# Optimization experiments

Hardware: AMD Instinct MI355X
Metric: run time of the kernel (lower is better)

The kernel has to match this reference:

```python
import jax, jax.numpy as jnp
import numpy as np

# ---- HashGrid config (tcnn defaults from module __init__) ----
N_LEVELS = 6
F = 2                      # n_features_per_level
T = 2 ** 19                # hashmap size
BASE = 16                  # base_resolution, per_level_scale=2.0
_RES = [BASE * (2 ** l) for l in range(N_LEVELS)]          # 16..512
_SIZES = [min(r ** 3, T) for r in _RES]                    # dense if grid fits
_OFFSETS = [0] + list(np.cumsum(_SIZES))
TOTAL_ENTRIES = int(_OFFSETS[-1])
_PRIMES = (1, 2654435761, 805459861)
BOX_R = 1.0
DIM_H = 64
DIM_IN = 3 + N_LEVELS * F


def hash_encode(xn, grid):
    """Multi-res hash-grid encoding. xn: [N,3] in [0,1]; grid: [TOTAL_ENTRIES, F]."""
    feats = []
    for l in range(N_LEVELS):
        res, size, off = _RES[l], _SIZES[l], _OFFSETS[l]
        dense = (res ** 3) <= T
        pos = xn * jnp.float32(res - 1) + 0.5          # tcnn: scale*x + 0.5
        pg = jnp.floor(pos)
        frac = pos - pg                                # [N,3]
        pgi = pg.astype(jnp.uint32)
        acc = jnp.zeros((xn.shape[0], F), xn.dtype)
        for corner in range(8):                        # trilinear, 8 corners
            cb = jnp.array([(corner >> d) & 1 for d in range(3)], dtype=jnp.uint32)
            c = pgi + cb                               # [N,3] corner coords
            w = jnp.prod(jnp.where(cb == 1, frac, 1.0 - frac), axis=-1)  # [N]
            if dense:
                c = jnp.minimum(c, jnp.uint32(res - 1))
                idx = c[:, 0] + c[:, 1] * jnp.uint32(res) + c[:, 2] * jnp.uint32(res * res)
            else:
                idx = ((c[:, 0] * jnp.uint32(_PRIMES[0]))
                       ^ (c[:, 1] * jnp.uint32(_PRIMES[1]))
                       ^ (c[:, 2] * jnp.uint32(_PRIMES[2]))) % jnp.uint32(size)
            acc = acc + w[:, None] * grid[jnp.uint32(off) + idx]
        feats.append(acc)
    return jnp.concatenate(feats, axis=-1)             # [N, 12]


def setup_inputs() -> dict:
    key = jax.random.key(0)
    k0, k1, k2 = jax.random.split(key, 3)
    N = 2_097_152
    x = jax.random.uniform(k0, (N, 3), jnp.float32, -1.0, 1.0)
    grid = jax.random.uniform(k1, (TOTAL_ENTRIES, F), jnp.float32, -1e-2, 1e-2)
    W0 = jax.random.normal(k2, (DIM_IN, DIM_H), jnp.float32) * float(np.sqrt(2.0 / DIM_H))
    b0 = jnp.zeros((DIM_H,), jnp.float32)
    W1 = jnp.full((DIM_H, 1), float(np.sqrt(np.pi / DIM_H)), jnp.float32)
    b1 = jnp.full((1,), -1.0, jnp.float32)             # -init_radius
    return {"x": x, "grid": grid, "W0": W0, "b0": b0, "W1": W1, "b1": b1}


def reference(x, grid, W0, b0, W1, b1):
    xn = (x + BOX_R) / (2.0 * BOX_R)                   # normalize to [0,1]
    f = hash_encode(xn, grid)                          # [N,12]
    h = jnp.concatenate([x, f], axis=-1)               # [N,15]
    h = jax.nn.relu(h @ W0 + b0)                       # [N,64]
    return h @ W1 + b1                                 # [N,1] scalar level s
```

## Files before the change

kernel.cpp:

```cpp
#include <hip/hip_runtime.h>


#define HP1 2654435761u
#define HP2 805459861u
#define HMASK ((1u << 19) - 1u)

typedef float v2f __attribute__((ext_vector_type(2)));

static __device__ __forceinline__ unsigned umin_(unsigned a, unsigned b) {
    return a < b ? a : b;
}

static __device__ __forceinline__ unsigned f2bf(float f) {
    unsigned u = __float_as_uint(f);
    return (u + 0x7fffu + ((u >> 16) & 1u)) >> 16;
}
static __device__ __forceinline__ float bf2f_lo(unsigned p) {
    return __uint_as_float((p & 0xffffu) << 16);
}
static __device__ __forceinline__ float bf2f_hi(unsigned p) {
    return __uint_as_float(p & 0xffff0000u);
}

static __device__ __forceinline__ v2f vmax0(v2f s) {
#if __has_builtin(__builtin_elementwise_max)
    return __builtin_elementwise_max(s, (v2f)0.0f);
#else
    v2f r; r.x = fmaxf(s.x, 0.0f); r.y = fmaxf(s.y, 0.0f); return r;
#endif
}

static __device__ __forceinline__ void hash_body(
    const float* __restrict__ x, const float2* __restrict__ tab,
    unsigned* __restrict__ feat, float scale, int N, int bid)
{
    const int gid = bid * 256 + threadIdx.x;
    if (gid >= N) return;

    const float px = __builtin_nontemporal_load(x + 3 * gid + 0);
    const float py = __builtin_nontemporal_load(x + 3 * gid + 1);
    const float pz = __builtin_nontemporal_load(x + 3 * gid + 2);

    const float p0 = fmaf((px + 1.0f) * 0.5f, scale, 0.5f);
    const float p1 = fmaf((py + 1.0f) * 0.5f, scale, 0.5f);
    const float p2 = fmaf((pz + 1.0f) * 0.5f, scale, 0.5f);
    const float g0 = floorf(p0), g1 = floorf(p1), g2 = floorf(p2);
    const float f0 = p0 - g0, f1 = p1 - g1, f2 = p2 - g2;
    const unsigned i0 = (unsigned)g0, i1 = (unsigned)g1, i2 = (unsigned)g2;

    const float wx[2] = {1.0f - f0, f0};
    const float wy[2] = {1.0f - f1, f1};
    const float wz[2] = {1.0f - f2, f2};
    const unsigned hx[2] = {i0, i0 + 1u};
    const unsigned hy[2] = {i1 * HP1, (i1 + 1u) * HP1};
    const unsigned hz[2] = {i2 * HP2, (i2 + 1u) * HP2};

    unsigned idx[8];
    float w[8];
    #pragma unroll
    for (int c = 0; c < 8; ++c) {
        const int bx = c & 1, by = (c >> 1) & 1, bz = (c >> 2) & 1;
        idx[c] = (hx[bx] ^ hy[by] ^ hz[bz]) & HMASK;
        w[c] = wx[bx] * wy[by] * wz[bz];
    }
    float2 v[8];
    #pragma unroll
    for (int c = 0; c < 8; ++c) v[c] = tab[idx[c]];

    float a0 = 0.0f, a1 = 0.0f;
    #pragma unroll
    for (int c = 0; c < 8; ++c) {
        a0 = fmaf(w[c], v[c].x, a0);
        a1 = fmaf(w[c], v[c].y, a1);
    }
    __builtin_nontemporal_store(f2bf(a0) | (f2bf(a1) << 16), feat + gid);
}

__global__ __launch_bounds__(256) void hash3_prep_kernel(
    const float* __restrict__ x, const float2* __restrict__ gtab,
    unsigned* __restrict__ feat0, int N,
    float* __restrict__ wt, unsigned* __restrict__ packed,
    const float* __restrict__ W0, const float* __restrict__ b0,
    const float* __restrict__ W1, const float* __restrict__ b1)
{
    const int nh = (int)gridDim.x - 64;
    if ((int)blockIdx.x >= nh) {
        const int pb = (int)blockIdx.x - nh;
        for (int t = pb * 256 + threadIdx.x; t < 36864; t += 64 * 256) {
            const float2 e = gtab[t];
            packed[t] = f2bf(e.x) | (f2bf(e.y) << 16);
        }
        if (pb == 0) {
            for (int t = threadIdx.x; t < 1024; t += 256) {
                const int j = t >> 4, i = t & 15;
                wt[t] = (i == 15) ? b0[j] : W0[i * 64 + j];
            }
            if (threadIdx.x < 64) wt[1024 + threadIdx.x] = W1[threadIdx.x];
            if (threadIdx.x == 0) wt[1088] = b1[0];
        }
        return;
    }
    hash_body(x, gtab + 299008u, feat0, 127.0f, N, (int)blockIdx.x);
}

__global__ __launch_bounds__(256) void hash_level_kernel(
    const float* __restrict__ x, const float2* __restrict__ tab,
    unsigned* __restrict__ feat, float scale, int N)
{
    hash_body(x, tab, feat, scale, N, (int)blockIdx.x);
}

static __device__ __forceinline__ void dense_level(
    const float2* __restrict__ tab, unsigned res,
    float xn0, float xn1, float xn2, float& o0, float& o1)
{
    const float scale = (float)(res - 1);
    const float p0 = fmaf(xn0, scale, 0.5f);
    const float p1 = fmaf(xn1, scale, 0.5f);
    const float p2 = fmaf(xn2, scale, 0.5f);
    const float g0 = floorf(p0), g1 = floorf(p1), g2 = floorf(p2);
    const float f0 = p0 - g0, f1 = p1 - g1, f2 = p2 - g2;
    const unsigned i0 = (unsigned)g0, i1 = (unsigned)g1, i2 = (unsigned)g2;

    const unsigned rm1 = res - 1u;
    const unsigned cx[2] = {umin_(i0, rm1), umin_(i0 + 1u, rm1)};
    const unsigned cy[2] = {umin_(i1, rm1) * res, umin_(i1 + 1u, rm1) * res};
    const unsigned cz[2] = {umin_(i2, rm1) * res * res,
                            umin_(i2 + 1u, rm1) * res * res};
    const float wx[2] = {1.0f - f0, f0};
    const float wy[2] = {1.0f - f1, f1};
    const float wz[2] = {1.0f - f2, f2};

    float a0 = 0.0f, a1 = 0.0f;
    #pragma unroll
    for (int c = 0; c < 8; ++c) {
        const int bx = c & 1, by = (c >> 1) & 1, bz = (c >> 2) & 1;
        const unsigned idx = cx[bx] + cy[by] + cz[bz];
        const float w = wx[bx] * wy[by] * wz[bz];
        const float2 v = tab[idx];
        a0 = fmaf(w, v.x, a0);
        a1 = fmaf(w, v.y, a1);
    }
    o0 = a0;
    o1 = a1;
}

static __device__ __forceinline__ void dense_level_lds(
    const unsigned* __restrict__ sPk, unsigned off, unsigned res,
    float xn0, float xn1, float xn2, float& o0, float& o1)
{
    const float scale = (float)(res - 1);
    const float p0 = fmaf(xn0, scale, 0.5f);
    const float p1 = fmaf(xn1, scale, 0.5f);
    const float p2 = fmaf(xn2, scale, 0.5f);
    const float g0 = floorf(p0), g1 = floorf(p1), g2 = floorf(p2);
    const float f0 = p0 - g0, f1 = p1 - g1, f2 = p2 - g2;
    const unsigned i0 = (unsigned)g0, i1 = (unsigned)g1, i2 = (unsigned)g2;

    const unsigned rm1 = res - 1u;
    const unsigned cx[2] = {umin_(i0, rm1), umin_(i0 + 1u, rm1)};
    const unsigned cy[2] = {umin_(i1, rm1) * res, umin_(i1 + 1u, rm1) * res};
    const unsigned cz[2] = {umin_(i2, rm1) * res * res,
                            umin_(i2 + 1u, rm1) * res * res};
    const float wx[2] = {1.0f - f0, f0};
    const float wy[2] = {1.0f - f1, f1};
    const float wz[2] = {1.0f - f2, f2};

    float a0 = 0.0f, a1 = 0.0f;
    #pragma unroll
    for (int c = 0; c < 8; ++c) {
        const int bx = c & 1, by = (c >> 1) & 1, bz = (c >> 2) & 1;
        const unsigned p = sPk[off + cx[bx] + cy[by] + cz[bz]];
        const float w = wx[bx] * wy[by] * wz[bz];
        a0 = fmaf(w, bf2f_lo(p), a0);
        a1 = fmaf(w, bf2f_hi(p), a1);
    }
    o0 = a0;
    o1 = a1;
}

template<int BLOCK, bool L1LDS>
__global__ __launch_bounds__(BLOCK, 4) void dense_mlp_kernel(
    const float* __restrict__ x,
    const float* __restrict__ grid,
    const unsigned* __restrict__ feat,
    const float* __restrict__ wt,
    const unsigned* __restrict__ packed,
    float* __restrict__ out, int N)
{
    extern __shared__ unsigned sPk[];
    const int tid = threadIdx.x;

    const int nstage = L1LDS ? 36864 : 4096;
    for (int t = tid; t < nstage; t += BLOCK)
        sPk[t] = packed[t];
    __syncthreads();

    const int base = blockIdx.x * (BLOCK * 4) + tid;
    const float2* gtab = (const float2*)grid;

    v2f hp[2][16];

    #pragma unroll
    for (int k = 0; k < 4; ++k) {
        const int g = base + BLOCK * k;
        const int gs = (g < N) ? g : 0;
        const int p = k >> 1, lane = k & 1;

        const float px = __builtin_nontemporal_load(x + 3 * gs + 0);
        const float py = __builtin_nontemporal_load(x + 3 * gs + 1);
        const float pz = __builtin_nontemporal_load(x + 3 * gs + 2);
        const float xn0 = (px + 1.0f) * 0.5f;
        const float xn1 = (py + 1.0f) * 0.5f;
        const float xn2 = (pz + 1.0f) * 0.5f;

        hp[p][0][lane] = px; hp[p][1][lane] = py; hp[p][2][lane] = pz;
        hp[p][15][lane] = 1.0f;

        float t3, t4, t5, t6, t7, t8;
        dense_level_lds(sPk, 0u, 16u, xn0, xn1, xn2, t3, t4);
        if (L1LDS)
            dense_level_lds(sPk, 4096u, 32u, xn0, xn1, xn2, t5, t6);
        else
            dense_level(gtab + 4096u, 32u, xn0, xn1, xn2, t5, t6);
        dense_level(gtab + 36864u, 64u, xn0, xn1, xn2, t7, t8);
        hp[p][3][lane] = t3; hp[p][4][lane] = t4;
        hp[p][5][lane] = t5; hp[p][6][lane] = t6;
        hp[p][7][lane] = t7; hp[p][8][lane] = t8;

        #pragma unroll
        for (int l = 0; l < 3; ++l) {
            const unsigned pk = __builtin_nontemporal_load(
                feat + (size_t)l * N + gs);
            hp[p][9 + 2 * l][lane]  = bf2f_lo(pk);
            hp[p][10 + 2 * l][lane] = bf2f_hi(pk);
        }
    }

    const float b1v = wt[1088];
    v2f o2[2];
    o2[0] = (v2f)b1v; o2[1] = (v2f)b1v;

    #pragma unroll 4
    for (int j = 0; j < 64; ++j) {
        float r[16];
        #pragma unroll
        for (int i = 0; i < 16; ++i)
            r[i] = wt[j * 16 + i];
        const float w1j = wt[1024 + j];
        #pragma unroll
        for (int p = 0; p < 2; ++p) {
            v2f s = (v2f)0.0f;
            #pragma unroll
            for (int i = 0; i < 16; ++i)
                s = hp[p][i] * r[i] + s;
            s = vmax0(s);
            o2[p] = s * w1j + o2[p];
        }
    }

    #pragma unroll
    for (int k = 0; k < 4; ++k) {
        const int g = base + BLOCK * k;
        if (g < N)
            __builtin_nontemporal_store(o2[k >> 1][k & 1], out + g);
    }
}

extern "C" void kernel_launch(void* const* d_in, const int* in_sizes, int n_in,
                              void* d_out, int out_size, void* d_ws, size_t ws_size,
                              hipStream_t stream) {
    const float* x    = (const float*)d_in[0];
    const float* grid = (const float*)d_in[1];
    const float* W0   = (const float*)d_in[2];
    const float* b0   = (const float*)d_in[3];
    const float* W1   = (const float*)d_in[4];
    const float* b1   = (const float*)d_in[5];
    float* out = (float*)d_out;

    const int N = in_sizes[0] / 3;
    const int blocks1 = (N + 255) / 256;

    const float2* gtab = (const float2*)grid;

    auto align256 = [](size_t v) { return (v + 255) & ~(size_t)255; };
    size_t off = 0;
    const size_t feat_off = off; off += align256((size_t)3 * N * 4);
    const size_t wt_off   = off; off += align256(1089 * 4);
    const size_t pk_off   = off; off += align256(36864 * 4);
    (void)ws_size;

    unsigned* feat   = (unsigned*)((char*)d_ws + feat_off);
    float*    wt     = (float*)((char*)d_ws + wt_off);
    unsigned* packed = (unsigned*)((char*)d_ws + pk_off);

    hash3_prep_kernel<<<blocks1 + 64, 256, 0, stream>>>(
        x, gtab, feat + (size_t)0 * N, N, wt, packed, W0, b0, W1, b1);
    hash_level_kernel<<<blocks1, 256, 0, stream>>>(x, gtab + 823296u,
                                                   feat + (size_t)1 * N, 255.0f, N);
    hash_level_kernel<<<blocks1, 256, 0, stream>>>(x, gtab + 1347584u,
                                                   feat + (size_t)2 * N, 511.0f, N);

    const size_t bigShm = 36864u * 4u;
    const void* bigK =
        reinterpret_cast<const void*>(&dense_mlp_kernel<1024, true>);
    (void)hipFuncSetAttribute(bigK,
        hipFuncAttributeMaxDynamicSharedMemorySize, (int)bigShm);
    bool big = false;
    hipFuncAttributes fa{};
    if (hipFuncGetAttributes(&fa, bigK) == hipSuccess)
        big = ((size_t)fa.maxDynamicSharedSizeBytes >= bigShm);

    if (big) {
        const int blocksB = (N + 4095) / 4096;
        dense_mlp_kernel<1024, true><<<blocksB, 1024, bigShm, stream>>>(
            x, (const float*)grid, feat, wt, packed, out, N);
    } else {
        const int blocksF = (N + 1023) / 1024;
        dense_mlp_kernel<256, false><<<blocksF, 256, 4096u * 4u, stream>>>(
            x, (const float*)grid, feat, wt, packed, out, N);
    }
}
```

Measured before the change: 313.9 us.

## Fuse hashed-level lookups into the dense+MLP kernel, dropping feature buffer

The three hashed-level encodings now run inside the main dense+MLP kernel instead of in separate kernels that wrote bf16-packed features to a workspace buffer. The prep kernel only packs the dense tables and weights. This removes two launches and the write and read of 3*N packed features, and it keeps the hashed features in fp32. The cost is much higher register pressure and more random gathers per thread in a kernel that already holds 2x16 v2f activations, which may lower occupancy or cause spills. It also loses the cross-point overlap that separate kernels had.

After: 413.0 us. +31.6%, slower.

```diff
diff --git a/kernel.cpp b/kernel.cpp
--- a/kernel.cpp
+++ b/kernel.cpp
@@ -30,20 +30,13 @@
 #endif
 }
 
-static __device__ __forceinline__ void hash_body(
-    const float* __restrict__ x, const float2* __restrict__ tab,
-    unsigned* __restrict__ feat, float scale, int N, int bid)
-{
-    const int gid = bid * 256 + threadIdx.x;
-    if (gid >= N) return;
-
-    const float px = __builtin_nontemporal_load(x + 3 * gid + 0);
-    const float py = __builtin_nontemporal_load(x + 3 * gid + 1);
-    const float pz = __builtin_nontemporal_load(x + 3 * gid + 2);
-
-    const float p0 = fmaf((px + 1.0f) * 0.5f, scale, 0.5f);
-    const float p1 = fmaf((py + 1.0f) * 0.5f, scale, 0.5f);
-    const float p2 = fmaf((pz + 1.0f) * 0.5f, scale, 0.5f);
+static __device__ __forceinline__ void hash_level_pt(
+    const float2* __restrict__ tab, float xn0, float xn1, float xn2,
+    float scale, float& o0, float& o1)
+{
+    const float p0 = fmaf(xn0, scale, 0.5f);
+    const float p1 = fmaf(xn1, scale, 0.5f);
+    const float p2 = fmaf(xn2, scale, 0.5f);
     const float g0 = floorf(p0), g1 = floorf(p1), g2 = floorf(p2);
     const float f0 = p0 - g0, f1 = p1 - g1, f2 = p2 - g2;
     const unsigned i0 = (unsigned)g0, i1 = (unsigned)g1, i2 = (unsigned)g2;
@@ -73,41 +66,28 @@
         a0 = fmaf(w[c], v[c].x, a0);
         a1 = fmaf(w[c], v[c].y, a1);
     }
-    __builtin_nontemporal_store(f2bf(a0) | (f2bf(a1) << 16), feat + gid);
-}
-
-__global__ __launch_bounds__(256) void hash3_prep_kernel(
-    const float* __restrict__ x, const float2* __restrict__ gtab,
-    unsigned* __restrict__ feat0, int N,
+    o0 = a0;
+    o1 = a1;
+}
+
+__global__ __launch_bounds__(256) void prep_kernel(
+    const float2* __restrict__ gtab,
     float* __restrict__ wt, unsigned* __restrict__ packed,
     const float* __restrict__ W0, const float* __restrict__ b0,
     const float* __restrict__ W1, const float* __restrict__ b1)
 {
-    const int nh = (int)gridDim.x - 64;
-    if ((int)blockIdx.x >= nh) {
-        const int pb = (int)blockIdx.x - nh;
-        for (int t = pb * 256 + threadIdx.x; t < 36864; t += 64 * 256) {
-            const float2 e = gtab[t];
-            packed[t] = f2bf(e.x) | (f2bf(e.y) << 16);
+    for (int t = (int)blockIdx.x * 256 + threadIdx.x; t < 36864; t += 64 * 256) {
+        const float2 e = gtab[t];
+        packed[t] = f2bf(e.x) | (f2bf(e.y) << 16);
+    }
+    if (blockIdx.x == 0) {
+        for (int t = threadIdx.x; t < 1024; t += 256) {
+            const int j = t >> 4, i = t & 15;
+            wt[t] = (i == 15) ? b0[j] : W0[i * 64 + j];
         }
-        if (pb == 0) {
-            for (int t = threadIdx.x; t < 1024; t += 256) {
-                const int j = t >> 4, i = t & 15;
-                wt[t] = (i == 15) ? b0[j] : W0[i * 64 + j];
-            }
-            if (threadIdx.x < 64) wt[1024 + threadIdx.x] = W1[threadIdx.x];
-            if (threadIdx.x == 0) wt[1088] = b1[0];
-        }
-        return;
-    }
-    hash_body(x, gtab + 299008u, feat0, 127.0f, N, (int)blockIdx.x);
-}
-
-__global__ __launch_bounds__(256) void hash_level_kernel(
-    const float* __restrict__ x, const float2* __restrict__ tab,
-    unsigned* __restrict__ feat, float scale, int N)
-{
-    hash_body(x, tab, feat, scale, N, (int)blockIdx.x);
+        if (threadIdx.x < 64) wt[1024 + threadIdx.x] = W1[threadIdx.x];
+        if (threadIdx.x == 0) wt[1088] = b1[0];
+    }
 }
 
 static __device__ __forceinline__ void dense_level(
@@ -180,10 +160,9 @@
 }
 
 template<int BLOCK, bool L1LDS>
-__global__ __launch_bounds__(BLOCK, 4) void dense_mlp_kernel(
+__global__ __launch_bounds__(BLOCK, 4) void fused_kernel(
     const float* __restrict__ x,
     const float* __restrict__ grid,
-    const unsigned* __restrict__ feat,
     const float* __restrict__ wt,
     const unsigned* __restrict__ packed,
     float* __restrict__ out, int N)
@@ -228,13 +207,13 @@
         hp[p][5][lane] = t5; hp[p][6][lane] = t6;
         hp[p][7][lane] = t7; hp[p][8][lane] = t8;
 
-        #pragma unroll
-        for (int l = 0; l < 3; ++l) {
-            const unsigned pk = __builtin_nontemporal_load(
-                feat + (size_t)l * N + gs);
-            hp[p][9 + 2 * l][lane]  = bf2f_lo(pk);
-            hp[p][10 + 2 * l][lane] = bf2f_hi(pk);
-        }
+        float h3a, h3b, h4a, h4b, h5a, h5b;
+        hash_level_pt(gtab + 299008u,  xn0, xn1, xn2, 127.0f, h3a, h3b);
+        hash_level_pt(gtab + 823296u,  xn0, xn1, xn2, 255.0f, h4a, h4b);
+        hash_level_pt(gtab + 1347584u, xn0, xn1, xn2, 511.0f, h5a, h5b);
+        hp[p][9][lane]  = h3a; hp[p][10][lane] = h3b;
+        hp[p][11][lane] = h4a; hp[p][12][lane] = h4b;
+        hp[p][13][lane] = h5a; hp[p][14][lane] = h5b;
     }
 
     const float b1v = wt[1088];
@@ -279,31 +258,22 @@
     float* out = (float*)d_out;
 
     const int N = in_sizes[0] / 3;
-    const int blocks1 = (N + 255) / 256;
-
     const float2* gtab = (const float2*)grid;
 
     auto align256 = [](size_t v) { return (v + 255) & ~(size_t)255; };
     size_t off = 0;
-    const size_t feat_off = off; off += align256((size_t)3 * N * 4);
-    const size_t wt_off   = off; off += align256(1089 * 4);
-    const size_t pk_off   = off; off += align256(36864 * 4);
+    const size_t wt_off = off; off += align256(1089 * 4);
+    const size_t pk_off = off; off += align256(36864 * 4);
     (void)ws_size;
 
-    unsigned* feat   = (unsigned*)((char*)d_ws + feat_off);
     float*    wt     = (float*)((char*)d_ws + wt_off);
     unsigned* packed = (unsigned*)((char*)d_ws + pk_off);
 
-    hash3_prep_kernel<<<blocks1 + 64, 256, 0, stream>>>(
-        x, gtab, feat + (size_t)0 * N, N, wt, packed, W0, b0, W1, b1);
-    hash_level_kernel<<<blocks1, 256, 0, stream>>>(x, gtab + 823296u,
-                                                   feat + (size_t)1 * N, 255.0f, N);
-    hash_level_kernel<<<blocks1, 256, 0, stream>>>(x, gtab + 1347584u,
-                                                   feat + (size_t)2 * N, 511.0f, N);
+    prep_kernel<<<64, 256, 0, stream>>>(gtab, wt, packed, W0, b0, W1, b1);
 
     const size_t bigShm = 36864u * 4u;
     const void* bigK =
-        reinterpret_cast<const void*>(&dense_mlp_kernel<1024, true>);
+        reinterpret_cast<const void*>(&fused_kernel<1024, true>);
     (void)hipFuncSetAttribute(bigK,
         hipFuncAttributeMaxDynamicSharedMemorySize, (int)bigShm);
     bool big = false;
@@ -313,11 +283,11 @@
 
     if (big) {
         const int blocksB = (N + 4095) / 4096;
-        dense_mlp_kernel<1024, true><<<blocksB, 1024, bigShm, stream>>>(
-            x, (const float*)grid, feat, wt, packed, out, N);
+        fused_kernel<1024, true><<<blocksB, 1024, bigShm, stream>>>(
+            x, (const float*)grid, wt, packed, out, N);
     } else {
         const int blocksF = (N + 1023) / 1024;
-        dense_mlp_kernel<256, false><<<blocksF, 256, 4096u * 4u, stream>>>(
-            x, (const float*)grid, feat, wt, packed, out, N);
-    }
-}
+        fused_kernel<256, false><<<blocksF, 256, 4096u * 4u, stream>>>(
+            x, (const float*)grid, wt, packed, out, N);
+    }
+}
```

## Pair x-neighbor hash entries into vector loads and pack level-2 into bf16 pair tables

Applied to the files above, without the earlier changes.

In the hashed level-3 body, the x-corner pair (i0, i0^1) is fetched with one 16-byte load when i0 is even, with a fallback to separate loads for odd i0. This halves the gather count in the common case. For dense level 2 (res 64), the prep kernel now builds two bf16-packed tables, A2 and B2, where B2 holds each entry's x+1 neighbor. The MLP kernel can then fetch both x corners with one 8-byte load. The change adds prep work, 2MB of extra workspace, and bf16 rounding on level 2.

Result: slower. 369.9 us (+17.8%).

```diff
diff --git a/kernel.cpp b/kernel.cpp
--- a/kernel.cpp
+++ b/kernel.cpp
@@ -51,27 +51,40 @@
     const float wx[2] = {1.0f - f0, f0};
     const float wy[2] = {1.0f - f1, f1};
     const float wz[2] = {1.0f - f2, f2};
-    const unsigned hx[2] = {i0, i0 + 1u};
     const unsigned hy[2] = {i1 * HP1, (i1 + 1u) * HP1};
     const unsigned hz[2] = {i2 * HP2, (i2 + 1u) * HP2};
 
-    unsigned idx[8];
-    float w[8];
-    #pragma unroll
-    for (int c = 0; c < 8; ++c) {
-        const int bx = c & 1, by = (c >> 1) & 1, bz = (c >> 2) & 1;
-        idx[c] = (hx[bx] ^ hy[by] ^ hz[bz]) & HMASK;
-        w[c] = wx[bx] * wy[by] * wz[bz];
-    }
-    float2 v[8];
-    #pragma unroll
-    for (int c = 0; c < 8; ++c) v[c] = tab[idx[c]];
+    float2 v0[4], v1[4];
+    #pragma unroll
+    for (int c = 0; c < 4; ++c) {
+        const unsigned m = hy[c & 1] ^ hz[(c >> 1) & 1];
+        const unsigned e0 = (i0 ^ m) & HMASK;
+        const float4 q = *reinterpret_cast<const float4*>(
+            reinterpret_cast<const float*>(tab) + 2u * (e0 & ~1u));
+        const float2 qlo = make_float2(q.x, q.y);
+        const float2 qhi = make_float2(q.z, q.w);
+        const bool hi = (e0 & 1u) != 0u;
+        v0[c] = hi ? qhi : qlo;
+        v1[c] = hi ? qlo : qhi;
+    }
+    if (i0 & 1u) {
+        #pragma unroll
+        for (int c = 0; c < 4; ++c) {
+            const unsigned e1 =
+                ((i0 + 1u) ^ hy[c & 1] ^ hz[(c >> 1) & 1]) & HMASK;
+            v1[c] = tab[e1];
+        }
+    }
 
     float a0 = 0.0f, a1 = 0.0f;
     #pragma unroll
-    for (int c = 0; c < 8; ++c) {
-        a0 = fmaf(w[c], v[c].x, a0);
-        a1 = fmaf(w[c], v[c].y, a1);
+    for (int c = 0; c < 4; ++c) {
+        const float wyz = wy[c & 1] * wz[(c >> 1) & 1];
+        const float w0 = wyz * wx[0], w1 = wyz * wx[1];
+        a0 = fmaf(w0, v0[c].x, a0);
+        a1 = fmaf(w0, v0[c].y, a1);
+        a0 = fmaf(w1, v1[c].x, a0);
+        a1 = fmaf(w1, v1[c].y, a1);
     }
     __builtin_nontemporal_store(f2bf(a0) | (f2bf(a1) << 16), feat + gid);
 }
@@ -80,6 +93,7 @@
     const float* __restrict__ x, const float2* __restrict__ gtab,
     unsigned* __restrict__ feat0, int N,
     float* __restrict__ wt, unsigned* __restrict__ packed,
+    unsigned* __restrict__ A2, unsigned* __restrict__ B2,
     const float* __restrict__ W0, const float* __restrict__ b0,
     const float* __restrict__ W1, const float* __restrict__ b1)
 {
@@ -89,6 +103,14 @@
         for (int t = pb * 256 + threadIdx.x; t < 36864; t += 64 * 256) {
             const float2 e = gtab[t];
             packed[t] = f2bf(e.x) | (f2bf(e.y) << 16);
+        }
+        const float2* g2 = gtab + 36864u;
+        for (int t = pb * 256 + threadIdx.x; t < 262144; t += 64 * 256) {
+            const float2 e = g2[t];
+            A2[t] = f2bf(e.x) | (f2bf(e.y) << 16);
+            const int xc = t & 63;
+            const float2 en = g2[(xc == 63) ? t : t + 1];
+            B2[t] = f2bf(en.x) | (f2bf(en.y) << 16);
         }
         if (pb == 0) {
             for (int t = threadIdx.x; t < 1024; t += 256) {
@@ -145,6 +167,45 @@
     o1 = a1;
 }
 
+static __device__ __forceinline__ void dense_level2_pk(
+    const unsigned* __restrict__ A2, const unsigned* __restrict__ B2,
+    float xn0, float xn1, float xn2, float& o0, float& o1)
+{
+    const float p0 = fmaf(xn0, 63.0f, 0.5f);
+    const float p1 = fmaf(xn1, 63.0f, 0.5f);
+    const float p2 = fmaf(xn2, 63.0f, 0.5f);
+    const float g0 = floorf(p0), g1 = floorf(p1), g2 = floorf(p2);
+    const float f0 = p0 - g0, f1 = p1 - g1, f2 = p2 - g2;
+    const unsigned i0 = (unsigned)g0, i1 = (unsigned)g1, i2 = (unsigned)g2;
+
+    const unsigned cx0 = umin_(i0, 63u);
+    const unsigned cy[2] = {umin_(i1, 63u) * 64u, umin_(i1 + 1u, 63u) * 64u};
+    const unsigned cz[2] = {umin_(i2, 63u) * 4096u,
+                            umin_(i2 + 1u, 63u) * 4096u};
+    const float wx[2] = {1.0f - f0, f0};
+    const float wy[2] = {1.0f - f1, f1};
+    const float wz[2] = {1.0f - f2, f2};
+
+    const unsigned* tsel = (cx0 & 1u) ? B2 : A2;
+    const unsigned xb = cx0 & ~1u;
+
+    float a0 = 0.0f, a1 = 0.0f;
+    #pragma unroll
+    for (int c = 0; c < 4; ++c) {
+        const int by = c & 1, bz = (c >> 1) & 1;
+        const uint2 q = *reinterpret_cast<const uint2*>(
+            tsel + xb + cy[by] + cz[bz]);
+        const float wyz = wy[by] * wz[bz];
+        const float w0 = wyz * wx[0], w1 = wyz * wx[1];
+        a0 = fmaf(w0, bf2f_lo(q.x), a0);
+        a1 = fmaf(w0, bf2f_hi(q.x), a1);
+        a0 = fmaf(w1, bf2f_lo(q.y), a0);
+        a1 = fmaf(w1, bf2f_hi(q.y), a1);
+    }
+    o0 = a0;
+    o1 = a1;
+}
+
 static __device__ __forceinline__ void dense_level_lds(
     const unsigned* __restrict__ sPk, unsigned off, unsigned res,
     float xn0, float xn1, float xn2, float& o0, float& o1)
@@ -186,6 +247,8 @@
     const unsigned* __restrict__ feat,
     const float* __restrict__ wt,
     const unsigned* __restrict__ packed,
+    const unsigned* __restrict__ A2,
+    const unsigned* __restrict__ B2,
     float* __restrict__ out, int N)
 {
     extern __shared__ unsigned sPk[];
@@ -223,7 +286,7 @@
             dense_level_lds(sPk, 4096u, 32u, xn0, xn1, xn2, t5, t6);
         else
             dense_level(gtab + 4096u, 32u, xn0, xn1, xn2, t5, t6);
-        dense_level(gtab + 36864u, 64u, xn0, xn1, xn2, t7, t8);
+        dense_level2_pk(A2, B2, xn0, xn1, xn2, t7, t8);
         hp[p][3][lane] = t3; hp[p][4][lane] = t4;
         hp[p][5][lane] = t5; hp[p][6][lane] = t6;
         hp[p][7][lane] = t7; hp[p][8][lane] = t8;
@@ -288,14 +351,18 @@
     const size_t feat_off = off; off += align256((size_t)3 * N * 4);
     const size_t wt_off   = off; off += align256(1089 * 4);
     const size_t pk_off   = off; off += align256(36864 * 4);
+    const size_t a2_off   = off; off += align256(262144 * 4);
+    const size_t b2_off   = off; off += align256(262144 * 4);
     (void)ws_size;
 
     unsigned* feat   = (unsigned*)((char*)d_ws + feat_off);
     float*    wt     = (float*)((char*)d_ws + wt_off);
     unsigned* packed = (unsigned*)((char*)d_ws + pk_off);
+    unsigned* A2     = (unsigned*)((char*)d_ws + a2_off);
+    unsigned* B2     = (unsigned*)((char*)d_ws + b2_off);
 
     hash3_prep_kernel<<<blocks1 + 64, 256, 0, stream>>>(
-        x, gtab, feat + (size_t)0 * N, N, wt, packed, W0, b0, W1, b1);
+        x, gtab, feat + (size_t)0 * N, N, wt, packed, A2, B2, W0, b0, W1, b1);
     hash_level_kernel<<<blocks1, 256, 0, stream>>>(x, gtab + 823296u,
                                                    feat + (size_t)1 * N, 255.0f, N);
     hash_level_kernel<<<blocks1, 256, 0, stream>>>(x, gtab + 1347584u,
@@ -314,10 +381,10 @@
     if (big) {
         const int blocksB = (N + 4095) / 4096;
         dense_mlp_kernel<1024, true><<<blocksB, 1024, bigShm, stream>>>(
-            x, (const float*)grid, feat, wt, packed, out, N);
+            x, (const float*)grid, feat, wt, packed, A2, B2, out, N);
     } else {
         const int blocksF = (N + 1023) / 1024;
         dense_mlp_kernel<256, false><<<blocksF, 256, 4096u * 4u, stream>>>(
-            x, (const float*)grid, feat, wt, packed, out, N);
-    }
-}
+            x, (const float*)grid, feat, wt, packed, A2, B2, out, N);
+    }
+}
```

## Pack level-2 grid into paired bf16 tables and issue all gathers before MLP

Applied to the files above, without the earlier changes.

Level 2 (res 64) is converted in the prep kernel into two bf16-packed tables, A2 holding entry x and B2 holding entry x+1, so each y/z corner pair can be fetched with one 8-byte load selected by the parity of x. That replaces eight scattered float2 gathers with four uint2 loads. The dense kernel is also restructured to issue the x, level-2 and feature loads for all four points up front, then build features and run the MLP two points at a time, to overlap memory latency. The cost is 2 MB of extra workspace writes in the prep kernel, higher register pressure, and bf16 rounding on level 2.

After: 308.2 us. About the same (-1.8%).

```diff
diff --git a/kernel.cpp b/kernel.cpp
--- a/kernel.cpp
+++ b/kernel.cpp
@@ -80,6 +80,7 @@
     const float* __restrict__ x, const float2* __restrict__ gtab,
     unsigned* __restrict__ feat0, int N,
     float* __restrict__ wt, unsigned* __restrict__ packed,
+    unsigned* __restrict__ A2, unsigned* __restrict__ B2,
     const float* __restrict__ W0, const float* __restrict__ b0,
     const float* __restrict__ W1, const float* __restrict__ b1)
 {
@@ -89,6 +90,14 @@
         for (int t = pb * 256 + threadIdx.x; t < 36864; t += 64 * 256) {
             const float2 e = gtab[t];
             packed[t] = f2bf(e.x) | (f2bf(e.y) << 16);
+        }
+        const float2* g2 = gtab + 36864u;
+        for (int t = pb * 256 + threadIdx.x; t < 262144; t += 64 * 256) {
+            const float2 e = g2[t];
+            A2[t] = f2bf(e.x) | (f2bf(e.y) << 16);
+            const int xc = t & 63;
+            const float2 en = g2[(xc == 63) ? t : t + 1];
+            B2[t] = f2bf(en.x) | (f2bf(en.y) << 16);
         }
         if (pb == 0) {
             for (int t = threadIdx.x; t < 1024; t += 256) {
@@ -179,6 +188,111 @@
     o1 = a1;
 }
 
+
+static __device__ __forceinline__ void issue_point(
+    const float* __restrict__ x, const unsigned* __restrict__ A2,
+    const unsigned* __restrict__ B2, const unsigned* __restrict__ feat,
+    int gs, int N, float& px, float& py, float& pz,
+    uint2* __restrict__ q, unsigned* __restrict__ fw)
+{
+    px = __builtin_nontemporal_load(x + 3 * gs + 0);
+    py = __builtin_nontemporal_load(x + 3 * gs + 1);
+    pz = __builtin_nontemporal_load(x + 3 * gs + 2);
+    const float xn0 = (px + 1.0f) * 0.5f;
+    const float xn1 = (py + 1.0f) * 0.5f;
+    const float xn2 = (pz + 1.0f) * 0.5f;
+    const float p0 = fmaf(xn0, 63.0f, 0.5f);
+    const float p1 = fmaf(xn1, 63.0f, 0.5f);
+    const float p2 = fmaf(xn2, 63.0f, 0.5f);
+    const unsigned i0 = (unsigned)floorf(p0);
+    const unsigned i1 = (unsigned)floorf(p1);
+    const unsigned i2 = (unsigned)floorf(p2);
+    const unsigned cx0 = umin_(i0, 63u);
+    const unsigned cy0 = umin_(i1, 63u) * 64u, cy1 = umin_(i1 + 1u, 63u) * 64u;
+    const unsigned cz0 = umin_(i2, 63u) * 4096u,
+                   cz1 = umin_(i2 + 1u, 63u) * 4096u;
+    const unsigned* tsel = (cx0 & 1u) ? B2 : A2;
+    const unsigned xb = cx0 & ~1u;
+    q[0] = *reinterpret_cast<const uint2*>(tsel + xb + cy0 + cz0);
+    q[1] = *reinterpret_cast<const uint2*>(tsel + xb + cy1 + cz0);
+    q[2] = *reinterpret_cast<const uint2*>(tsel + xb + cy0 + cz1);
+    q[3] = *reinterpret_cast<const uint2*>(tsel + xb + cy1 + cz1);
+    fw[0] = __builtin_nontemporal_load(feat + (size_t)0 * N + gs);
+    fw[1] = __builtin_nontemporal_load(feat + (size_t)1 * N + gs);
+    fw[2] = __builtin_nontemporal_load(feat + (size_t)2 * N + gs);
+}
+
+template<bool L1LDS>
+static __device__ __forceinline__ void build_point(
+    const unsigned* __restrict__ sPk, const float2* __restrict__ gtab,
+    float px, float py, float pz,
+    const uint2* __restrict__ q, const unsigned* __restrict__ fw,
+    v2f* __restrict__ hp, int lane)
+{
+    const float xn0 = (px + 1.0f) * 0.5f;
+    const float xn1 = (py + 1.0f) * 0.5f;
+    const float xn2 = (pz + 1.0f) * 0.5f;
+    hp[0][lane] = px; hp[1][lane] = py; hp[2][lane] = pz;
+    hp[15][lane] = 1.0f;
+
+    float t3, t4, t5, t6;
+    dense_level_lds(sPk, 0u, 16u, xn0, xn1, xn2, t3, t4);
+    if (L1LDS)
+        dense_level_lds(sPk, 4096u, 32u, xn0, xn1, xn2, t5, t6);
+    else
+        dense_level(gtab + 4096u, 32u, xn0, xn1, xn2, t5, t6);
+    hp[3][lane] = t3; hp[4][lane] = t4;
+    hp[5][lane] = t5; hp[6][lane] = t6;
+
+    const float p0 = fmaf(xn0, 63.0f, 0.5f);
+    const float p1 = fmaf(xn1, 63.0f, 0.5f);
+    const float p2 = fmaf(xn2, 63.0f, 0.5f);
+    const float f0 = p0 - floorf(p0);
+    const float f1 = p1 - floorf(p1);
+    const float f2 = p2 - floorf(p2);
+    const float wx0 = 1.0f - f0, wx1 = f0;
+    const float wy[2] = {1.0f - f1, f1};
+    const float wz[2] = {1.0f - f2, f2};
+    float a0 = 0.0f, a1 = 0.0f;
+    #pragma unroll
+    for (int c = 0; c < 4; ++c) {
+        const float wyz = wy[c & 1] * wz[(c >> 1) & 1];
+        const float w0 = wyz * wx0, w1 = wyz * wx1;
+        a0 = fmaf(w0, bf2f_lo(q[c].x), a0);
+        a1 = fmaf(w0, bf2f_hi(q[c].x), a1);
+        a0 = fmaf(w1, bf2f_lo(q[c].y), a0);
+        a1 = fmaf(w1, bf2f_hi(q[c].y), a1);
+    }
+    hp[7][lane] = a0; hp[8][lane] = a1;
+
+    #pragma unroll
+    for (int l = 0; l < 3; ++l) {
+        hp[9 + 2 * l][lane]  = bf2f_lo(fw[l]);
+        hp[10 + 2 * l][lane] = bf2f_hi(fw[l]);
+    }
+}
+
+static __device__ __forceinline__ v2f mlp_pair(
+    const float* __restrict__ wt, const v2f* __restrict__ hp)
+{
+    v2f o2 = (v2f)wt[1088];
+    #pragma unroll 4
+    for (int j = 0; j < 64; ++j) {
+        float r[16];
+        #pragma unroll
+        for (int i = 0; i < 16; ++i)
+            r[i] = wt[j * 16 + i];
+        const float w1j = wt[1024 + j];
+        v2f s = (v2f)0.0f;
+        #pragma unroll
+        for (int i = 0; i < 16; ++i)
+            s = hp[i] * r[i] + s;
+        s = vmax0(s);
+        o2 = s * w1j + o2;
+    }
+    return o2;
+}
+
 template<int BLOCK, bool L1LDS>
 __global__ __launch_bounds__(BLOCK, 4) void dense_mlp_kernel(
     const float* __restrict__ x,
@@ -186,6 +300,8 @@
     const unsigned* __restrict__ feat,
     const float* __restrict__ wt,
     const unsigned* __restrict__ packed,
+    const unsigned* __restrict__ A2,
+    const unsigned* __restrict__ B2,
     float* __restrict__ out, int N)
 {
     extern __shared__ unsigned sPk[];
@@ -199,71 +315,32 @@
     const int base = blockIdx.x * (BLOCK * 4) + tid;
     const float2* gtab = (const float2*)grid;
 
-    v2f hp[2][16];
-
+    float px[4], py[4], pz[4];
+    uint2 q2[4][4];
+    unsigned fw[4][3];
     #pragma unroll
     for (int k = 0; k < 4; ++k) {
         const int g = base + BLOCK * k;
         const int gs = (g < N) ? g : 0;
-        const int p = k >> 1, lane = k & 1;
-
-        const float px = __builtin_nontemporal_load(x + 3 * gs + 0);
-        const float py = __builtin_nontemporal_load(x + 3 * gs + 1);
-        const float pz = __builtin_nontemporal_load(x + 3 * gs + 2);
-        const float xn0 = (px + 1.0f) * 0.5f;
-        const float xn1 = (py + 1.0f) * 0.5f;
-        const float xn2 = (pz + 1.0f) * 0.5f;
-
-        hp[p][0][lane] = px; hp[p][1][lane] = py; hp[p][2][lane] = pz;
-        hp[p][15][lane] = 1.0f;
-
-        float t3, t4, t5, t6, t7, t8;
-        dense_level_lds(sPk, 0u, 16u, xn0, xn1, xn2, t3, t4);
-        if (L1LDS)
-            dense_level_lds(sPk, 4096u, 32u, xn0, xn1, xn2, t5, t6);
-        else
-            dense_level(gtab + 4096u, 32u, xn0, xn1, xn2, t5, t6);
-        dense_level(gtab + 36864u, 64u, xn0, xn1, xn2, t7, t8);
-        hp[p][3][lane] = t3; hp[p][4][lane] = t4;
-        hp[p][5][lane] = t5; hp[p][6][lane] = t6;
-        hp[p][7][lane] = t7; hp[p][8][lane] = t8;
-
-        #pragma unroll
-        for (int l = 0; l < 3; ++l) {
-            const unsigned pk = __builtin_nontemporal_load(
-                feat + (size_t)l * N + gs);
-            hp[p][9 + 2 * l][lane]  = bf2f_lo(pk);
-            hp[p][10 + 2 * l][lane] = bf2f_hi(pk);
-        }
-    }
-
-    const float b1v = wt[1088];
-    v2f o2[2];
-    o2[0] = (v2f)b1v; o2[1] = (v2f)b1v;
-
-    #pragma unroll 4
-    for (int j = 0; j < 64; ++j) {
-        float r[16];
-        #pragma unroll
-        for (int i = 0; i < 16; ++i)
-            r[i] = wt[j * 16 + i];
-        const float w1j = wt[1024 + j];
-        #pragma unroll
-        for (int p = 0; p < 2; ++p) {
-            v2f s = (v2f)0.0f;
-            #pragma unroll
-            for (int i = 0; i < 16; ++i)
-                s = hp[p][i] * r[i] + s;
-            s = vmax0(s);
-            o2[p] = s * w1j + o2[p];
-        }
-    }
+        issue_point(x, A2, B2, feat, gs, N,
+                    px[k], py[k], pz[k], q2[k], fw[k]);
+    }
+
+    v2f hp[16];
+    build_point<L1LDS>(sPk, gtab, px[0], py[0], pz[0], q2[0], fw[0], hp, 0);
+    build_point<L1LDS>(sPk, gtab, px[1], py[1], pz[1], q2[1], fw[1], hp, 1);
+    const v2f oA = mlp_pair(wt, hp);
+    build_point<L1LDS>(sPk, gtab, px[2], py[2], pz[2], q2[2], fw[2], hp, 0);
+    build_point<L1LDS>(sPk, gtab, px[3], py[3], pz[3], q2[3], fw[3], hp, 1);
+    const v2f oB = mlp_pair(wt, hp);
 
     #pragma unroll
     for (int k = 0; k < 4; ++k) {
         const int g = base + BLOCK * k;
-        if (g < N)
-            __builtin_nontemporal_store(o2[k >> 1][k & 1], out + g);
+        if (g < N) {
+            const float o = (k < 2) ? oA[k & 1] : oB[k & 1];
+            __builtin_nontemporal_store(o, out + g);
+        }
     }
 }
 
@@ -288,18 +365,22 @@
     const size_t feat_off = off; off += align256((size_t)3 * N * 4);
     const size_t wt_off   = off; off += align256(1089 * 4);
     const size_t pk_off   = off; off += align256(36864 * 4);
+    const size_t a2_off   = off; off += align256(262144 * 4);
+    const size_t b2_off   = off; off += align256(262144 * 4);
     (void)ws_size;
 
     unsigned* feat   = (unsigned*)((char*)d_ws + feat_off);
     float*    wt     = (float*)((char*)d_ws + wt_off);
     unsigned* packed = (unsigned*)((char*)d_ws + pk_off);
+    unsigned* A2     = (unsigned*)((char*)d_ws + a2_off);
+    unsigned* B2     = (unsigned*)((char*)d_ws + b2_off);
 
     hash3_prep_kernel<<<blocks1 + 64, 256, 0, stream>>>(
-        x, gtab, feat + (size_t)0 * N, N, wt, packed, W0, b0, W1, b1);
-    hash_level_kernel<<<blocks1, 256, 0, stream>>>(x, gtab + 823296u,
-                                                   feat + (size_t)1 * N, 255.0f, N);
-    hash_level_kernel<<<blocks1, 256, 0, stream>>>(x, gtab + 1347584u,
-                                                   feat + (size_t)2 * N, 511.0f, N);
+        x, gtab, feat + (size_t)0 * N, N, wt, packed, A2, B2, W0, b0, W1, b1);
+    hash_level_kernel<<<blocks1, 256, 0, stream>>>(
+        x, gtab + 823296u, feat + (size_t)1 * N, 255.0f, N);
+    hash_level_kernel<<<blocks1, 256, 0, stream>>>(
+        x, gtab + 1347584u, feat + (size_t)2 * N, 511.0f, N);
 
     const size_t bigShm = 36864u * 4u;
     const void* bigK =
@@ -314,10 +395,10 @@
     if (big) {
         const int blocksB = (N + 4095) / 4096;
         dense_mlp_kernel<1024, true><<<blocksB, 1024, bigShm, stream>>>(
-            x, (const float*)grid, feat, wt, packed, out, N);
+            x, (const float*)grid, feat, wt, packed, A2, B2, out, N);
     } else {
         const int blocksF = (N + 1023) / 1024;
         dense_mlp_kernel<256, false><<<blocksF, 256, 4096u * 4u, stream>>>(
-            x, (const float*)grid, feat, wt, packed, out, N);
-    }
-}
+            x, (const float*)grid, feat, wt, packed, A2, B2, out, N);
+    }
+}
```
